# Kernel optimization log

Measured on AMD Instinct MI355X. Metric: run time of the kernel, lower is better.

## Reference

```python
import jax, jax.numpy as jnp
import numpy as np

IN_FEATURES = 4096
OUT_FEATURES = 4096
ACTIVE_IN = 1024
ACTIVE_OUT = 1024
BATCH, SEQ = 4, 2048


def setup_inputs() -> dict:
    key = jax.random.key(0)
    kx, kw, kb = jax.random.split(key, 3)
    x = jax.random.normal(kx, (BATCH, SEQ, IN_FEATURES), dtype=jnp.float32)
    # nn.Linear default init scale ~ 1/sqrt(fan_in)
    W = jax.random.normal(kw, (ACTIVE_OUT, ACTIVE_IN), dtype=jnp.float32) / np.sqrt(ACTIVE_IN)
    b = jax.random.normal(kb, (ACTIVE_OUT,), dtype=jnp.float32) / np.sqrt(ACTIVE_IN)
    rng = np.random.default_rng(42)
    # unique sorted index subsets (faithful to pruning-style selection; scatter is write-once)
    in_idx = jnp.asarray(np.sort(rng.choice(IN_FEATURES, ACTIVE_IN, replace=False)), dtype=jnp.int32)
    out_idx = jnp.asarray(np.sort(rng.choice(OUT_FEATURES, ACTIVE_OUT, replace=False)), dtype=jnp.int32)
    return {"x": x, "W": W, "b": b, "in_idx": in_idx, "out_idx": out_idx}


def reference(x, W, b, in_idx, out_idx):
    # gather active input columns: [B, S, ACTIVE_IN]
    x_active = jnp.take(x, in_idx, axis=-1)
    # dense linear: y = x_active @ W.T + b -> [B, S, ACTIVE_OUT]
    y = jnp.einsum('bsi,oi->bso', x_active, W) + b
    # scatter into zero-initialized full output buffer: [B, S, OUT_FEATURES]
    out = jnp.zeros(x.shape[:-1] + (OUT_FEATURES,), dtype=y.dtype)
    out = out.at[..., out_idx].set(y)
    return out
```

## Files before the change

### kernel.cpp

```cpp
#include <hip/hip_runtime.h>
#include <hip/hip_bf16.h>


typedef unsigned short u16;
typedef u16   u16x4 __attribute__((ext_vector_type(4)));
typedef u16   u16x8 __attribute__((ext_vector_type(8)));
typedef int   i32x4 __attribute__((ext_vector_type(4)));
typedef float f32x4 __attribute__((ext_vector_type(4)));
typedef __bf16 bf16x8 __attribute__((ext_vector_type(8)));

constexpr int IN_F  = 4096;
constexpr int OUT_F = 4096;
constexpr int AI    = 1024;
constexpr int AO    = 1024;
constexpr int M_ROWS = 4 * 2048;
constexpr int BM = 32;
constexpr int BK = 64;
constexpr int NTHREADS = 512;

__device__ __forceinline__ u16 f2bf(float f) {
    union { __hip_bfloat16 h; u16 u; } cv;
    cv.h = __float2bfloat16(f);
    return cv.u;
}

__global__ void prep_kernel(const float* __restrict__ W,
                            const int* __restrict__ out_idx,
                            u16* __restrict__ Wb, int* __restrict__ pos) {
    int t = blockIdx.x * blockDim.x + threadIdx.x;
    if (t < AO) pos[out_idx[t]] = t;
    f32x4 w = reinterpret_cast<const f32x4*>(W)[t];
    u16x4 v;
    v.x = f2bf(w.x); v.y = f2bf(w.y); v.z = f2bf(w.z); v.w = f2bf(w.w);
    reinterpret_cast<u16x4*>(Wb)[t] = v;
}

__global__ void gather_kernel(const float* __restrict__ x,
                              const int* __restrict__ in_idx,
                              u16* __restrict__ Xa) {
    int t = blockIdx.x * blockDim.x + threadIdx.x;
    int m  = t >> 7;
    int kc = (t & 127) * 8;
    const float* xr = x + (size_t)m * IN_F;
    u16x8 v;
#pragma unroll
    for (int j = 0; j < 8; ++j) v[j] = f2bf(xr[in_idx[kc + j]]);
    *reinterpret_cast<u16x8*>(Xa + (size_t)m * AI + kc) = v;
}

template <bool PRE>
__global__ __launch_bounds__(NTHREADS, 1)
void gemm_kernel(const float* __restrict__ x,
                 const u16* __restrict__ Xa,
                 const u16* __restrict__ Wb,
                 const float* __restrict__ bias,
                 const int* __restrict__ in_idx,
                 const int* __restrict__ pos,
                 float* __restrict__ out) {
    __shared__ u16 As[2][BM][BK + 8];
    __shared__ float ys[BM][AO + 1];

    const int tid  = threadIdx.x;
    const int wid  = tid >> 6;
    const int lane = tid & 63;
    const int n_lo = lane & 15;
    const int kg   = lane >> 4;
    const int m_base = blockIdx.x * BM;

    float bv[8];
#pragma unroll
    for (int f = 0; f < 8; ++f) bv[f] = bias[wid * 128 + f * 16 + n_lo];

    f32x4 acc[2][8];
#pragma unroll
    for (int mf = 0; mf < 2; ++mf)
#pragma unroll
        for (int f = 0; f < 8; ++f) acc[mf][f] = (f32x4)0.0f;

    const int srow = tid >> 4;
    const int sc4  = (tid & 15) * 4;

    auto stage = [&](int buf, int k0) {
        if constexpr (PRE) {
            const u16* src = Xa + (size_t)(m_base + srow) * AI + k0 + sc4;
            *reinterpret_cast<u16x4*>(&As[buf][srow][sc4]) =
                *reinterpret_cast<const u16x4*>(src);
        } else {
            const float* xr = x + (size_t)(m_base + srow) * IN_F;
            u16x4 v;
#pragma unroll
            for (int j = 0; j < 4; ++j) v[j] = f2bf(xr[in_idx[k0 + sc4 + j]]);
            *reinterpret_cast<u16x4*>(&As[buf][srow][sc4]) = v;
        }
    };

    stage(0, 0);
    int buf = 0;
    for (int kt = 0; kt < AI / BK; ++kt) {
        __syncthreads();
        if (kt + 1 < AI / BK) stage(buf ^ 1, (kt + 1) * BK);
        const int k0 = kt * BK;
#pragma unroll
        for (int kk = 0; kk < BK; kk += 32) {
            bf16x8 a[2];
            a[0] = *reinterpret_cast<const bf16x8*>(&As[buf][n_lo][kk + kg * 8]);
            a[1] = *reinterpret_cast<const bf16x8*>(&As[buf][16 + n_lo][kk + kg * 8]);
#pragma unroll
            for (int f = 0; f < 8; ++f) {
                const int n = wid * 128 + f * 16 + n_lo;
                bf16x8 bfr = *reinterpret_cast<const bf16x8*>(
                    Wb + (size_t)n * AI + k0 + kk + kg * 8);
                acc[0][f] = __builtin_amdgcn_mfma_f32_16x16x32_bf16(a[0], bfr, acc[0][f], 0, 0, 0);
                acc[1][f] = __builtin_amdgcn_mfma_f32_16x16x32_bf16(a[1], bfr, acc[1][f], 0, 0, 0);
            }
        }
        buf ^= 1;
    }

    __syncthreads();
#pragma unroll
    for (int mf = 0; mf < 2; ++mf)
#pragma unroll
        for (int f = 0; f < 8; ++f)
#pragma unroll
            for (int r = 0; r < 4; ++r)
                ys[mf * 16 + kg * 4 + r][wid * 128 + f * 16 + n_lo] =
                    acc[mf][f][r] + bv[f];
    __syncthreads();

    for (int i = tid; i < BM * (OUT_F / 4); i += NTHREADS) {
        int m  = i >> 10;
        int o4 = i & 1023;
        i32x4 p = reinterpret_cast<const i32x4*>(pos)[o4];
        f32x4 v;
        v.x = (p.x >= 0) ? ys[m][p.x] : 0.0f;
        v.y = (p.y >= 0) ? ys[m][p.y] : 0.0f;
        v.z = (p.z >= 0) ? ys[m][p.z] : 0.0f;
        v.w = (p.w >= 0) ? ys[m][p.w] : 0.0f;
        reinterpret_cast<f32x4*>(out + (size_t)(m_base + m) * OUT_F)[o4] = v;
    }
}

extern "C" void kernel_launch(void* const* d_in, const int* in_sizes, int n_in,
                              void* d_out, int out_size, void* d_ws, size_t ws_size,
                              hipStream_t stream) {
    const float* x      = (const float*)d_in[0];
    const float* W      = (const float*)d_in[1];
    const float* b      = (const float*)d_in[2];
    const int*   in_idx = (const int*)d_in[3];
    const int*   out_idx= (const int*)d_in[4];
    float* out = (float*)d_out;

    char* ws = (char*)d_ws;
    int* pos = (int*)ws;
    u16* Wb  = (u16*)(ws + 16384);
    u16* Xa  = (u16*)(ws + 16384 + 2 * 1024 * 1024);
    const size_t NEED_FULL = 16384 + 2u * 1024 * 1024 + (size_t)M_ROWS * AI * 2;

    hipMemsetAsync(pos, 0xFF, OUT_F * sizeof(int), stream);
    prep_kernel<<<1024, 256, 0, stream>>>(W, out_idx, Wb, pos);

    if (ws_size >= NEED_FULL) {
        gather_kernel<<<(M_ROWS * AI / 8) / 256, 256, 0, stream>>>(x, in_idx, Xa);
        gemm_kernel<true><<<M_ROWS / BM, NTHREADS, 0, stream>>>(x, Xa, Wb, b, in_idx, pos, out);
    } else {
        gemm_kernel<false><<<M_ROWS / BM, NTHREADS, 0, stream>>>(x, Xa, Wb, b, in_idx, pos, out);
    }
}
```

Baseline: 313.3 us.

## Restructure into LDS-staged gather, 128x128 tiled GEMM, and in-place scatter expand

```diff
diff --git a/kernel.cpp b/kernel.cpp
--- a/kernel.cpp
+++ b/kernel.cpp
@@ -4,7 +4,6 @@
 
 typedef unsigned short u16;
 typedef u16   u16x4 __attribute__((ext_vector_type(4)));
-typedef u16   u16x8 __attribute__((ext_vector_type(8)));
 typedef int   i32x4 __attribute__((ext_vector_type(4)));
 typedef float f32x4 __attribute__((ext_vector_type(4)));
 typedef __bf16 bf16x8 __attribute__((ext_vector_type(8)));
@@ -14,9 +13,7 @@
 constexpr int AI    = 1024;
 constexpr int AO    = 1024;
 constexpr int M_ROWS = 4 * 2048;
-constexpr int BM = 32;
-constexpr int BK = 64;
-constexpr int NTHREADS = 512;
+constexpr int NT_K  = AI / 64;
 
 __device__ __forceinline__ u16 f2bf(float f) {
     union { __hip_bfloat16 h; u16 u; } cv;
@@ -35,109 +32,147 @@
     reinterpret_cast<u16x4*>(Wb)[t] = v;
 }
 
-__global__ void gather_kernel(const float* __restrict__ x,
-                              const int* __restrict__ in_idx,
-                              u16* __restrict__ Xa) {
-    int t = blockIdx.x * blockDim.x + threadIdx.x;
-    int m  = t >> 7;
-    int kc = (t & 127) * 8;
-    const float* xr = x + (size_t)m * IN_F;
-    u16x8 v;
-#pragma unroll
-    for (int j = 0; j < 8; ++j) v[j] = f2bf(xr[in_idx[kc + j]]);
-    *reinterpret_cast<u16x8*>(Xa + (size_t)m * AI + kc) = v;
+__global__ __launch_bounds__(256)
+void gather_kernel(const float* __restrict__ x,
+                   const int* __restrict__ in_idx,
+                   u16* __restrict__ Xa) {
+    __shared__ float xrow[IN_F];
+    const int m = blockIdx.x;
+    const int t = threadIdx.x;
+    const f32x4* src = reinterpret_cast<const f32x4*>(x + (size_t)m * IN_F);
+#pragma unroll
+    for (int i = 0; i < 4; ++i)
+        *reinterpret_cast<f32x4*>(&xrow[i * 1024 + t * 4]) = src[i * 256 + t];
+    __syncthreads();
+    i32x4 idx = reinterpret_cast<const i32x4*>(in_idx)[t];
+    u16x4 v;
+    v.x = f2bf(xrow[idx.x]);
+    v.y = f2bf(xrow[idx.y]);
+    v.z = f2bf(xrow[idx.z]);
+    v.w = f2bf(xrow[idx.w]);
+    reinterpret_cast<u16x4*>(Xa + (size_t)m * AI)[t] = v;
 }
 
 template <bool PRE>
-__global__ __launch_bounds__(NTHREADS, 1)
-void gemm_kernel(const float* __restrict__ x,
-                 const u16* __restrict__ Xa,
-                 const u16* __restrict__ Wb,
-                 const float* __restrict__ bias,
-                 const int* __restrict__ in_idx,
-                 const int* __restrict__ pos,
-                 float* __restrict__ out) {
-    __shared__ u16 As[2][BM][BK + 8];
-    __shared__ float ys[BM][AO + 1];
-
+__global__ __launch_bounds__(256, 2)
+void gemm128(const float* __restrict__ x, const u16* __restrict__ Xa,
+             const u16* __restrict__ Wb, const float* __restrict__ bias,
+             const int* __restrict__ in_idx, float* __restrict__ out) {
+    __shared__ u16 As[2][128 * 64];
+    __shared__ u16 Bs[2][128 * 64];
     const int tid  = threadIdx.x;
     const int wid  = tid >> 6;
     const int lane = tid & 63;
     const int n_lo = lane & 15;
     const int kg   = lane >> 4;
-    const int m_base = blockIdx.x * BM;
-
-    float bv[8];
-#pragma unroll
-    for (int f = 0; f < 8; ++f) bv[f] = bias[wid * 128 + f * 16 + n_lo];
-
-    f32x4 acc[2][8];
-#pragma unroll
-    for (int mf = 0; mf < 2; ++mf)
-#pragma unroll
-        for (int f = 0; f < 8; ++f) acc[mf][f] = (f32x4)0.0f;
-
-    const int srow = tid >> 4;
-    const int sc4  = (tid & 15) * 4;
+    const int orig = blockIdx.x;
+    const int wgid = (orig & 7) * 64 + (orig >> 3);
+    const int mb = wgid >> 3, nb = wgid & 7;
+    const int m0 = mb * 128, n0 = nb * 128;
+    const int wm = wid >> 1, wn = wid & 1;
 
     auto stage = [&](int buf, int k0) {
         if constexpr (PRE) {
-            const u16* src = Xa + (size_t)(m_base + srow) * AI + k0 + sc4;
-            *reinterpret_cast<u16x4*>(&As[buf][srow][sc4]) =
-                *reinterpret_cast<const u16x4*>(src);
+            const int r8 = lane >> 3;
+            const int c8 = (lane & 7) * 8;
+#pragma unroll
+            for (int c = 0; c < 4; ++c) {
+                const int row = wid * 32 + c * 8;
+                __builtin_amdgcn_global_load_lds(
+                    (const __attribute__((address_space(1))) void*)
+                        (Xa + (size_t)(m0 + row + r8) * AI + k0 + c8),
+                    (__attribute__((address_space(3))) void*)&As[buf][row * 64],
+                    16, 0, 0);
+                __builtin_amdgcn_global_load_lds(
+                    (const __attribute__((address_space(1))) void*)
+                        (Wb + (size_t)(n0 + row + r8) * AI + k0 + c8),
+                    (__attribute__((address_space(3))) void*)&Bs[buf][row * 64],
+                    16, 0, 0);
+            }
         } else {
-            const float* xr = x + (size_t)(m_base + srow) * IN_F;
-            u16x4 v;
-#pragma unroll
-            for (int j = 0; j < 4; ++j) v[j] = f2bf(xr[in_idx[k0 + sc4 + j]]);
-            *reinterpret_cast<u16x4*>(&As[buf][srow][sc4]) = v;
+            const int rr = tid >> 1;
+            const int cc = (tid & 1) * 32;
+#pragma unroll
+            for (int j4 = 0; j4 < 32; j4 += 4) {
+                u16x4 va;
+#pragma unroll
+                for (int j = 0; j < 4; ++j)
+                    va[j] = f2bf(x[(size_t)(m0 + rr) * IN_F + in_idx[k0 + cc + j4 + j]]);
+                *reinterpret_cast<u16x4*>(&As[buf][rr * 64 + cc + j4]) = va;
+                *reinterpret_cast<u16x4*>(&Bs[buf][rr * 64 + cc + j4]) =
+                    *reinterpret_cast<const u16x4*>(Wb + (size_t)(n0 + rr) * AI + k0 + cc + j4);
+            }
         }
     };
 
+    f32x4 acc[4][4];
+#pragma unroll
+    for (int i = 0; i < 4; ++i)
+#pragma unroll
+        for (int j = 0; j < 4; ++j) acc[i][j] = (f32x4)0.0f;
+
     stage(0, 0);
     int buf = 0;
-    for (int kt = 0; kt < AI / BK; ++kt) {
+    for (int kt = 0; kt < NT_K; ++kt) {
         __syncthreads();
-        if (kt + 1 < AI / BK) stage(buf ^ 1, (kt + 1) * BK);
-        const int k0 = kt * BK;
-#pragma unroll
-        for (int kk = 0; kk < BK; kk += 32) {
-            bf16x8 a[2];
-            a[0] = *reinterpret_cast<const bf16x8*>(&As[buf][n_lo][kk + kg * 8]);
-            a[1] = *reinterpret_cast<const bf16x8*>(&As[buf][16 + n_lo][kk + kg * 8]);
-#pragma unroll
-            for (int f = 0; f < 8; ++f) {
-                const int n = wid * 128 + f * 16 + n_lo;
-                bf16x8 bfr = *reinterpret_cast<const bf16x8*>(
-                    Wb + (size_t)n * AI + k0 + kk + kg * 8);
-                acc[0][f] = __builtin_amdgcn_mfma_f32_16x16x32_bf16(a[0], bfr, acc[0][f], 0, 0, 0);
-                acc[1][f] = __builtin_amdgcn_mfma_f32_16x16x32_bf16(a[1], bfr, acc[1][f], 0, 0, 0);
-            }
+        if (kt + 1 < NT_K) stage(buf ^ 1, (kt + 1) * 64);
+#pragma unroll
+        for (int kk = 0; kk < 64; kk += 32) {
+            bf16x8 a[4], b[4];
+#pragma unroll
+            for (int i = 0; i < 4; ++i)
+                a[i] = *reinterpret_cast<const bf16x8*>(
+                    &As[buf][(wm * 64 + i * 16 + n_lo) * 64 + kk + kg * 8]);
+#pragma unroll
+            for (int j = 0; j < 4; ++j)
+                b[j] = *reinterpret_cast<const bf16x8*>(
+                    &Bs[buf][(wn * 64 + j * 16 + n_lo) * 64 + kk + kg * 8]);
+#pragma unroll
+            for (int i = 0; i < 4; ++i)
+#pragma unroll
+                for (int j = 0; j < 4; ++j)
+                    acc[i][j] = __builtin_amdgcn_mfma_f32_16x16x32_bf16(
+                        a[i], b[j], acc[i][j], 0, 0, 0);
         }
         buf ^= 1;
     }
 
+    float bv[4];
+#pragma unroll
+    for (int j = 0; j < 4; ++j) bv[j] = bias[n0 + wn * 64 + j * 16 + n_lo];
+#pragma unroll
+    for (int i = 0; i < 4; ++i) {
+        const int gm = m0 + wm * 64 + i * 16 + kg * 4;
+#pragma unroll
+        for (int j = 0; j < 4; ++j) {
+            const int gn = n0 + wn * 64 + j * 16 + n_lo;
+#pragma unroll
+            for (int r = 0; r < 4; ++r)
+                out[(size_t)(gm + r) * OUT_F + gn] = acc[i][j][r] + bv[j];
+        }
+    }
+}
+
+__global__ __launch_bounds__(256)
+void expand_kernel(const int* __restrict__ pos, float* __restrict__ out) {
+    __shared__ float yrow[AO];
+    const int m = blockIdx.x;
+    const int t = threadIdx.x;
+    float* row = out + (size_t)m * OUT_F;
+    *reinterpret_cast<f32x4*>(&yrow[t * 4]) =
+        *reinterpret_cast<const f32x4*>(row + t * 4);
     __syncthreads();
-#pragma unroll
-    for (int mf = 0; mf < 2; ++mf)
-#pragma unroll
-        for (int f = 0; f < 8; ++f)
-#pragma unroll
-            for (int r = 0; r < 4; ++r)
-                ys[mf * 16 + kg * 4 + r][wid * 128 + f * 16 + n_lo] =
-                    acc[mf][f][r] + bv[f];
-    __syncthreads();
-
-    for (int i = tid; i < BM * (OUT_F / 4); i += NTHREADS) {
-        int m  = i >> 10;
-        int o4 = i & 1023;
-        i32x4 p = reinterpret_cast<const i32x4*>(pos)[o4];
+    const i32x4* pos4 = reinterpret_cast<const i32x4*>(pos);
+#pragma unroll
+    for (int c = 0; c < 4; ++c) {
+        const int o4 = c * 256 + t;
+        i32x4 p = pos4[o4];
         f32x4 v;
-        v.x = (p.x >= 0) ? ys[m][p.x] : 0.0f;
-        v.y = (p.y >= 0) ? ys[m][p.y] : 0.0f;
-        v.z = (p.z >= 0) ? ys[m][p.z] : 0.0f;
-        v.w = (p.w >= 0) ? ys[m][p.w] : 0.0f;
-        reinterpret_cast<f32x4*>(out + (size_t)(m_base + m) * OUT_F)[o4] = v;
+        v.x = (p.x >= 0) ? yrow[p.x] : 0.0f;
+        v.y = (p.y >= 0) ? yrow[p.y] : 0.0f;
+        v.z = (p.z >= 0) ? yrow[p.z] : 0.0f;
+        v.w = (p.w >= 0) ? yrow[p.w] : 0.0f;
+        *reinterpret_cast<f32x4*>(row + o4 * 4) = v;
     }
 }
 
@@ -161,9 +196,12 @@
     prep_kernel<<<1024, 256, 0, stream>>>(W, out_idx, Wb, pos);
 
     if (ws_size >= NEED_FULL) {
-        gather_kernel<<<(M_ROWS * AI / 8) / 256, 256, 0, stream>>>(x, in_idx, Xa);
-        gemm_kernel<true><<<M_ROWS / BM, NTHREADS, 0, stream>>>(x, Xa, Wb, b, in_idx, pos, out);
+        gather_kernel<<<M_ROWS, 256, 0, stream>>>(x, in_idx, Xa);
+        gemm128<true><<<(M_ROWS / 128) * (AO / 128), 256, 0, stream>>>(
+            x, Xa, Wb, b, in_idx, out);
     } else {
-        gemm_kernel<false><<<M_ROWS / BM, NTHREADS, 0, stream>>>(x, Xa, Wb, b, in_idx, pos, out);
-    }
-}
+        gemm128<false><<<(M_ROWS / 128) * (AO / 128), 256, 0, stream>>>(
+            x, Xa, Wb, b, in_idx, out);
+    }
+    expand_kernel<<<M_ROWS, 256, 0, stream>>>(pos, out);
+}
```

New measurement: 281.6 us. 10.1% less time.

## Restructure gather via LDS row staging and GEMM with full-K LDS tile, bf16 epilogue

Applied to the files above, without the earlier changes.

```diff
diff --git a/kernel.cpp b/kernel.cpp
--- a/kernel.cpp
+++ b/kernel.cpp
@@ -4,7 +4,6 @@
 
 typedef unsigned short u16;
 typedef u16   u16x4 __attribute__((ext_vector_type(4)));
-typedef u16   u16x8 __attribute__((ext_vector_type(8)));
 typedef int   i32x4 __attribute__((ext_vector_type(4)));
 typedef float f32x4 __attribute__((ext_vector_type(4)));
 typedef __bf16 bf16x8 __attribute__((ext_vector_type(8)));
@@ -14,14 +13,17 @@
 constexpr int AI    = 1024;
 constexpr int AO    = 1024;
 constexpr int M_ROWS = 4 * 2048;
-constexpr int BM = 32;
-constexpr int BK = 64;
-constexpr int NTHREADS = 512;
+constexpr int BM    = 16;
 
 __device__ __forceinline__ u16 f2bf(float f) {
     union { __hip_bfloat16 h; u16 u; } cv;
     cv.h = __float2bfloat16(f);
     return cv.u;
+}
+__device__ __forceinline__ float bf2f(u16 u) {
+    union { float f; unsigned int i; } cv;
+    cv.i = ((unsigned int)u) << 16;
+    return cv.f;
 }
 
 __global__ void prep_kernel(const float* __restrict__ W,
@@ -35,109 +37,111 @@
     reinterpret_cast<u16x4*>(Wb)[t] = v;
 }
 
-__global__ void gather_kernel(const float* __restrict__ x,
-                              const int* __restrict__ in_idx,
-                              u16* __restrict__ Xa) {
-    int t = blockIdx.x * blockDim.x + threadIdx.x;
-    int m  = t >> 7;
-    int kc = (t & 127) * 8;
-    const float* xr = x + (size_t)m * IN_F;
-    u16x8 v;
+__global__ __launch_bounds__(256)
+void gather_kernel(const float* __restrict__ x,
+                   const int* __restrict__ in_idx,
+                   u16* __restrict__ Xa) {
+    __shared__ float xrow[IN_F];
+    const int m = blockIdx.x;
+    const int t = threadIdx.x;
+    const f32x4* src = reinterpret_cast<const f32x4*>(x + (size_t)m * IN_F);
 #pragma unroll
-    for (int j = 0; j < 8; ++j) v[j] = f2bf(xr[in_idx[kc + j]]);
-    *reinterpret_cast<u16x8*>(Xa + (size_t)m * AI + kc) = v;
+    for (int i = 0; i < 4; ++i)
+        *reinterpret_cast<f32x4*>(&xrow[i * 1024 + t * 4]) = src[i * 256 + t];
+    __syncthreads();
+    i32x4 idx = reinterpret_cast<const i32x4*>(in_idx)[t];
+    u16x4 v;
+    v.x = f2bf(xrow[idx.x]);
+    v.y = f2bf(xrow[idx.y]);
+    v.z = f2bf(xrow[idx.z]);
+    v.w = f2bf(xrow[idx.w]);
+    reinterpret_cast<u16x4*>(Xa + (size_t)m * AI)[t] = v;
 }
 
-template <bool PRE>
-__global__ __launch_bounds__(NTHREADS, 1)
-void gemm_kernel(const float* __restrict__ x,
-                 const u16* __restrict__ Xa,
-                 const u16* __restrict__ Wb,
-                 const float* __restrict__ bias,
-                 const int* __restrict__ in_idx,
-                 const int* __restrict__ pos,
-                 float* __restrict__ out) {
-    __shared__ u16 As[2][BM][BK + 8];
-    __shared__ float ys[BM][AO + 1];
+union TileU {
+    u16 As[BM][1024];
+    u16 ys[BM][1040];
+    char bytes[BM * 1040 * 2];
+};
 
-    const int tid  = threadIdx.x;
-    const int wid  = tid >> 6;
-    const int lane = tid & 63;
+__global__ __launch_bounds__(512, 4)
+void gemmx_kernel(const u16* __restrict__ Xa, const u16* __restrict__ Wb,
+                  const float* __restrict__ bias, const int* __restrict__ pos,
+                  float* __restrict__ out) {
+    __shared__ TileU L;
+    const int t    = threadIdx.x;
+    const int wid  = t >> 6;
+    const int lane = t & 63;
     const int n_lo = lane & 15;
     const int kg   = lane >> 4;
-    const int m_base = blockIdx.x * BM;
+    const int m0   = blockIdx.x * BM;
+
+#pragma unroll
+    for (int c = 0; c < 4; ++c) {
+        const int flat = c * 8192 + t * 16;
+        const int row  = flat >> 11;
+        const int colb = flat & 2047;
+        const int scolb = colb ^ ((row & 15) << 4);
+        const u16* src = Xa + (size_t)(m0 + row) * AI + (scolb >> 1);
+        __builtin_amdgcn_global_load_lds(
+            (const __attribute__((address_space(1))) void*)src,
+            (__attribute__((address_space(3))) void*)(L.bytes + c * 8192 + (wid << 10)),
+            16, 0, 0);
+    }
 
     float bv[8];
 #pragma unroll
     for (int f = 0; f < 8; ++f) bv[f] = bias[wid * 128 + f * 16 + n_lo];
 
-    f32x4 acc[2][8];
+    f32x4 acc[8];
 #pragma unroll
-    for (int mf = 0; mf < 2; ++mf)
+    for (int f = 0; f < 8; ++f) acc[f] = (f32x4)0.0f;
+
+    __syncthreads();
+
+    const u16* wbase = Wb + (size_t)(wid * 128 + n_lo) * AI + kg * 8;
+#pragma unroll 2
+    for (int kk = 0; kk < AI; kk += 32) {
+        const int cb = kk * 2 + kg * 16;
+        bf16x8 a = *reinterpret_cast<const bf16x8*>(
+            L.bytes + (n_lo << 11) + (cb ^ (n_lo << 4)));
+        bf16x8 b0, b1, b2, b3;
 #pragma unroll
-        for (int f = 0; f < 8; ++f) acc[mf][f] = (f32x4)0.0f;
-
-    const int srow = tid >> 4;
-    const int sc4  = (tid & 15) * 4;
-
-    auto stage = [&](int buf, int k0) {
-        if constexpr (PRE) {
-            const u16* src = Xa + (size_t)(m_base + srow) * AI + k0 + sc4;
-            *reinterpret_cast<u16x4*>(&As[buf][srow][sc4]) =
-                *reinterpret_cast<const u16x4*>(src);
-        } else {
-            const float* xr = x + (size_t)(m_base + srow) * IN_F;
-            u16x4 v;
-#pragma unroll
-            for (int j = 0; j < 4; ++j) v[j] = f2bf(xr[in_idx[k0 + sc4 + j]]);
-            *reinterpret_cast<u16x4*>(&As[buf][srow][sc4]) = v;
+        for (int h = 0; h < 2; ++h) {
+            const u16* wp = wbase + (size_t)(h * 4 * 16) * AI + kk;
+            b0 = *reinterpret_cast<const bf16x8*>(wp);
+            b1 = *reinterpret_cast<const bf16x8*>(wp + (size_t)16 * AI);
+            b2 = *reinterpret_cast<const bf16x8*>(wp + (size_t)32 * AI);
+            b3 = *reinterpret_cast<const bf16x8*>(wp + (size_t)48 * AI);
+            acc[h * 4 + 0] = __builtin_amdgcn_mfma_f32_16x16x32_bf16(a, b0, acc[h * 4 + 0], 0, 0, 0);
+            acc[h * 4 + 1] = __builtin_amdgcn_mfma_f32_16x16x32_bf16(a, b1, acc[h * 4 + 1], 0, 0, 0);
+            acc[h * 4 + 2] = __builtin_amdgcn_mfma_f32_16x16x32_bf16(a, b2, acc[h * 4 + 2], 0, 0, 0);
+            acc[h * 4 + 3] = __builtin_amdgcn_mfma_f32_16x16x32_bf16(a, b3, acc[h * 4 + 3], 0, 0, 0);
         }
-    };
-
-    stage(0, 0);
-    int buf = 0;
-    for (int kt = 0; kt < AI / BK; ++kt) {
-        __syncthreads();
-        if (kt + 1 < AI / BK) stage(buf ^ 1, (kt + 1) * BK);
-        const int k0 = kt * BK;
-#pragma unroll
-        for (int kk = 0; kk < BK; kk += 32) {
-            bf16x8 a[2];
-            a[0] = *reinterpret_cast<const bf16x8*>(&As[buf][n_lo][kk + kg * 8]);
-            a[1] = *reinterpret_cast<const bf16x8*>(&As[buf][16 + n_lo][kk + kg * 8]);
-#pragma unroll
-            for (int f = 0; f < 8; ++f) {
-                const int n = wid * 128 + f * 16 + n_lo;
-                bf16x8 bfr = *reinterpret_cast<const bf16x8*>(
-                    Wb + (size_t)n * AI + k0 + kk + kg * 8);
-                acc[0][f] = __builtin_amdgcn_mfma_f32_16x16x32_bf16(a[0], bfr, acc[0][f], 0, 0, 0);
-                acc[1][f] = __builtin_amdgcn_mfma_f32_16x16x32_bf16(a[1], bfr, acc[1][f], 0, 0, 0);
-            }
-        }
-        buf ^= 1;
     }
 
     __syncthreads();
+
 #pragma unroll
-    for (int mf = 0; mf < 2; ++mf)
+    for (int f = 0; f < 8; ++f)
 #pragma unroll
-        for (int f = 0; f < 8; ++f)
-#pragma unroll
-            for (int r = 0; r < 4; ++r)
-                ys[mf * 16 + kg * 4 + r][wid * 128 + f * 16 + n_lo] =
-                    acc[mf][f][r] + bv[f];
+        for (int r = 0; r < 4; ++r)
+            L.ys[kg * 4 + r][wid * 128 + f * 16 + n_lo] = f2bf(acc[f][r] + bv[f]);
     __syncthreads();
 
-    for (int i = tid; i < BM * (OUT_F / 4); i += NTHREADS) {
-        int m  = i >> 10;
-        int o4 = i & 1023;
-        i32x4 p = reinterpret_cast<const i32x4*>(pos)[o4];
+    const i32x4* pos4 = reinterpret_cast<const i32x4*>(pos);
+#pragma unroll 4
+    for (int it = 0; it < 32; ++it) {
+        const int idx = it * 512 + t;
+        const int row = idx >> 10;
+        const int o4  = idx & 1023;
+        i32x4 p = pos4[o4];
         f32x4 v;
-        v.x = (p.x >= 0) ? ys[m][p.x] : 0.0f;
-        v.y = (p.y >= 0) ? ys[m][p.y] : 0.0f;
-        v.z = (p.z >= 0) ? ys[m][p.z] : 0.0f;
-        v.w = (p.w >= 0) ? ys[m][p.w] : 0.0f;
-        reinterpret_cast<f32x4*>(out + (size_t)(m_base + m) * OUT_F)[o4] = v;
+        v.x = (p.x >= 0) ? bf2f(L.ys[row][p.x]) : 0.0f;
+        v.y = (p.y >= 0) ? bf2f(L.ys[row][p.y]) : 0.0f;
+        v.z = (p.z >= 0) ? bf2f(L.ys[row][p.z]) : 0.0f;
+        v.w = (p.w >= 0) ? bf2f(L.ys[row][p.w]) : 0.0f;
+        reinterpret_cast<f32x4*>(out + (size_t)(m0 + row) * OUT_F)[o4] = v;
     }
 }
 
@@ -155,15 +159,9 @@
     int* pos = (int*)ws;
     u16* Wb  = (u16*)(ws + 16384);
     u16* Xa  = (u16*)(ws + 16384 + 2 * 1024 * 1024);
-    const size_t NEED_FULL = 16384 + 2u * 1024 * 1024 + (size_t)M_ROWS * AI * 2;
 
     hipMemsetAsync(pos, 0xFF, OUT_F * sizeof(int), stream);
     prep_kernel<<<1024, 256, 0, stream>>>(W, out_idx, Wb, pos);
-
-    if (ws_size >= NEED_FULL) {
-        gather_kernel<<<(M_ROWS * AI / 8) / 256, 256, 0, stream>>>(x, in_idx, Xa);
-        gemm_kernel<true><<<M_ROWS / BM, NTHREADS, 0, stream>>>(x, Xa, Wb, b, in_idx, pos, out);
-    } else {
-        gemm_kernel<false><<<M_ROWS / BM, NTHREADS, 0, stream>>>(x, Xa, Wb, b, in_idx, pos, out);
-    }
+    gather_kernel<<<M_ROWS, 256, 0, stream>>>(x, in_idx, Xa);
+    gemmx_kernel<<<M_ROWS / BM, 512, 0, stream>>>(Xa, Wb, b, pos, out);
 }
```

Measured after the change: 356.2 us. +13.7%, slower.
